# Performance work log

Measured on AMD Instinct MI355X. Metric: run time of the kernel, lower is better.

Reference implementation:

```python
import jax, jax.numpy as jnp
import numpy as np

B_NW, N, DIM, NH, DH, HID, NW, WH = 2048, 64, 512, 16, 32, 384, 64, 8
EPS = 1e-12  # F.normalize eps

def _rel_coords_log(wh, ww):
    # torch.cartesian_prod order: i (rows) outer, j (cols) inner
    ii, jj = np.meshgrid(np.arange(wh), np.arange(ww), indexing='ij')
    coords = np.stack([ii.ravel(), jj.ravel()], axis=-1).astype(np.float32)  # [N,2]
    rel = coords[:, None, :] - coords[None, :, :]                            # [N,N,2]
    return (np.sign(rel) * np.log1p(np.abs(rel))).astype(np.float32)

def setup_inputs() -> dict:
    key = jax.random.key(0)
    ks = jax.random.split(key, 9)
    s = 0.02
    inner = NH * DH
    return {
        'x': jax.random.normal(ks[0], (B_NW, N, DIM), jnp.float32),
        'mask': jax.random.normal(ks[1], (NW, N, N), jnp.float32),
        'w_qkv': jax.random.normal(ks[2], (DIM, 3 * inner), jnp.float32) * s,
        'tau': jnp.ones((1, NH, 1, 1), jnp.float32),
        'mlp_w1': jax.random.normal(ks[3], (2, HID), jnp.float32) * s,
        'mlp_b1': jnp.zeros((HID,), jnp.float32),
        'mlp_w2': jax.random.normal(ks[4], (HID, NH), jnp.float32) * s,
        'mlp_b2': jnp.zeros((NH,), jnp.float32),
        'w_out': jax.random.normal(ks[5], (inner, DIM), jnp.float32) * s,
        'b_out': jnp.zeros((DIM,), jnp.float32),
        'rel_log': jnp.asarray(_rel_coords_log(WH, WH)),
    }

def reference(x, mask, w_qkv, tau, mlp_w1, mlp_b1, mlp_w2, mlp_b2, w_out, b_out, rel_log):
    b, n, _ = x.shape
    qkv = x @ w_qkv                                   # [b, n, 3*nh*dh]
    qkv = qkv.reshape(b, n, 3, NH, DH)
    q, k, v = (jnp.transpose(qkv[:, :, i], (0, 2, 1, 3)) for i in range(3))  # [b, nh, n, dh]
    # cosine attention: L2-normalize q and k along head dim
    q = q / jnp.maximum(jnp.linalg.norm(q, axis=-1, keepdims=True), EPS)
    k = k / jnp.maximum(jnp.linalg.norm(k, axis=-1, keepdims=True), EPS)
    sim = jnp.einsum('bhid,bhjd->bhij', q, k) * tau   # learned temperature
    # relative position bias via meta MLP: [N,N,2] -> [N,N,nh]
    bias = jax.nn.relu(rel_log @ mlp_w1 + mlp_b1) @ mlp_w2 + mlp_b2
    sim = sim + jnp.transpose(bias, (2, 0, 1))[None]  # [1, nh, N, N]
    nw = mask.shape[0]
    sim = sim.reshape(b // nw, nw, NH, n, n) + mask[None, :, None]
    sim = sim.reshape(b, NH, n, n)
    attn = jax.nn.softmax(sim, axis=-1)
    out = jnp.einsum('bhij,bhjd->bhid', attn, v)
    out = jnp.transpose(out, (0, 2, 1, 3)).reshape(b, n, NH * DH)
    return out @ w_out + b_out
```

## Files before the change

### kernel.cpp

```cpp
#include <hip/hip_runtime.h>
#include <hip/hip_bf16.h>


typedef __bf16 bf16;
typedef __bf16 v4bf __attribute__((ext_vector_type(4)));
typedef __bf16 v8bf __attribute__((ext_vector_type(8)));
typedef float  v4f  __attribute__((ext_vector_type(4)));

__global__ void convert_x_kernel(const float* __restrict__ x, bf16* __restrict__ xbf) {
    const int stride = gridDim.x * 256;
    for (size_t idx = blockIdx.x * 256 + threadIdx.x; idx < 8388608; idx += stride) {
        const float4* xv = (const float4*)x;
        float4 v0 = xv[idx * 2];
        float4 v1 = xv[idx * 2 + 1];
        v8bf o = { (bf16)v0.x, (bf16)v0.y, (bf16)v0.z, (bf16)v0.w,
                   (bf16)v1.x, (bf16)v1.y, (bf16)v1.z, (bf16)v1.w };
        *(v8bf*)(xbf + idx * 8) = o;
    }
}

__global__ void convert_w_kernel(const float* __restrict__ wqkv, const float* __restrict__ wout,
                                 bf16* __restrict__ Wt, bf16* __restrict__ WoT) {
    int idx = blockIdx.x * 256 + threadIdx.x;
    Wt[idx] = (bf16)wqkv[(idx & 511) * 1536 + (idx >> 9)];
    if (idx < 262144) WoT[idx] = (bf16)wout[(idx & 511) * 512 + (idx >> 9)];
}

__global__ void bias_kernel(const float* __restrict__ rel_log, const float* __restrict__ w1,
                            const float* __restrict__ b1, const float* __restrict__ w2,
                            const float* __restrict__ b2, float* __restrict__ bias) {
    int p = blockIdx.x * 256 + threadIdx.x;
    float ra = rel_log[p * 2 + 0];
    float rb = rel_log[p * 2 + 1];
    float acc[16];
    #pragma unroll
    for (int t = 0; t < 16; ++t) acc[t] = 0.f;
    for (int kk = 0; kk < 384; ++kk) {
        float hv = fmaxf(ra * w1[kk] + rb * w1[384 + kk] + b1[kk], 0.f);
        #pragma unroll
        for (int t = 0; t < 16; ++t) acc[t] += hv * w2[kk * 16 + t];
    }
    #pragma unroll
    for (int t = 0; t < 16; ++t) bias[t * 4096 + p] = acc[t] + b2[t];
}

__global__ void comb_kernel(const float* __restrict__ bias, const float* __restrict__ mask,
                            float* __restrict__ comb) {
    int idx = blockIdx.x * 256 + threadIdx.x;
    int t = idx & 4095, wh = idx >> 12;
    int w = wh >> 4, h = wh & 15;
    int ji = t >> 8, rem = t & 255;
    int j = ji >> 2, i = ji & 3;
    int q16 = rem >> 2, r = t & 3;
    int lq = q16 >> 4, lm = q16 & 15;
    int p = (i * 16 + lm) * 64 + j * 16 + lq * 4 + r;
    comb[idx] = bias[h * 4096 + p] + mask[w * 4096 + p];
}

__global__ __launch_bounds__(256) void qkv_gemm_kernel(
    const bf16* __restrict__ xbf,
    const bf16* __restrict__ Wt,
    bf16* __restrict__ q_ws, bf16* __restrict__ k_ws, bf16* __restrict__ v_ws)
{
    __shared__ alignas(16) bf16 Alds[2][128 * 32];
    __shared__ alignas(16) bf16 Blds[2][128 * 32];
    const int bid = blockIdx.x, nwg = gridDim.x;
    const int wid = (bid & 7) * (nwg >> 3) + (bid >> 3);
    const int nb = wid % 12, mb = wid / 12;

    const int t = threadIdx.x;
    const int wv = t >> 6, lane = t & 63, lq = lane >> 4, lm = lane & 15;
    const int wr = wv >> 1, wc = wv & 1;

    const char* aBase = (const char*)xbf + (size_t)mb * 128 * 1024;
    const char* bBase = (const char*)Wt + (size_t)nb * 128 * 1024;

    auto stage = [&](int buf, int kt) {
        #pragma unroll
        for (int p = 0; p < 2; ++p) {
            int idx = (p * 4 + wv) * 1024 + lane * 16;
            int row = idx >> 6, kb = idx & 63;
            __builtin_amdgcn_global_load_lds(
                (const __attribute__((address_space(1))) void*)(aBase + (size_t)row * 1024 + kt * 64 + kb),
                (__attribute__((address_space(3))) void*)((char*)Alds + buf * 8192 + (p * 4 + wv) * 1024),
                16, 0, 0);
            __builtin_amdgcn_global_load_lds(
                (const __attribute__((address_space(1))) void*)(bBase + (size_t)row * 1024 + kt * 64 + kb),
                (__attribute__((address_space(3))) void*)((char*)Blds + buf * 8192 + (p * 4 + wv) * 1024),
                16, 0, 0);
        }
    };

    v4f acc[4][4];
    #pragma unroll
    for (int i = 0; i < 4; ++i)
        #pragma unroll
        for (int j = 0; j < 4; ++j) acc[i][j] = v4f{0.f, 0.f, 0.f, 0.f};

    stage(0, 0);
    #pragma unroll 1
    for (int kt = 0; kt < 16; ++kt) {
        if (kt < 15) {
            stage((kt + 1) & 1, kt + 1);
            asm volatile("s_waitcnt vmcnt(4)" ::: "memory");
        } else {
            asm volatile("s_waitcnt vmcnt(0)" ::: "memory");
        }
        __builtin_amdgcn_s_barrier();
        __builtin_amdgcn_sched_barrier(0);
        const bf16* Ab = &Alds[kt & 1][0];
        const bf16* Bb = &Blds[kt & 1][0];
        v8bf af[4], bfj[4];
        #pragma unroll
        for (int i = 0; i < 4; ++i)
            af[i] = *(const v8bf*)(Ab + (wr * 64 + i * 16 + lm) * 32 + lq * 8);
        #pragma unroll
        for (int j = 0; j < 4; ++j)
            bfj[j] = *(const v8bf*)(Bb + (wc * 64 + j * 16 + lm) * 32 + lq * 8);
        #pragma unroll
        for (int i = 0; i < 4; ++i)
            #pragma unroll
            for (int j = 0; j < 4; ++j)
                acc[i][j] = __builtin_amdgcn_mfma_f32_16x16x32_bf16(af[i], bfj[j], acc[i][j], 0, 0, 0);
        __builtin_amdgcn_s_barrier();
    }

    const int bw = mb * 2 + wr;
    if (nb < 8) {
        bf16* dst = (nb < 4) ? q_ws : k_ws;
        const int hbase = (nb & 3) * 4 + wc * 2;
        #pragma unroll
        for (int tpair = 0; tpair < 2; ++tpair) {
            const int h = hbase + tpair;
            #pragma unroll
            for (int i = 0; i < 4; ++i)
                #pragma unroll
                for (int r = 0; r < 4; ++r) {
                    int n = i * 16 + lq * 4 + r;
                    size_t base = ((size_t)(bw * 16 + h) * 64 + n) * 32;
                    dst[base + lm]      = (bf16)acc[i][2 * tpair][r];
                    dst[base + 16 + lm] = (bf16)acc[i][2 * tpair + 1][r];
                }
        }
    } else {
        #pragma unroll
        for (int j = 0; j < 4; ++j) {
            const int h = (nb - 8) * 4 + wc * 2 + (j >> 1);
            const int dh = (j & 1) * 16 + lm;
            #pragma unroll
            for (int i = 0; i < 4; ++i) {
                v4bf pv = { (bf16)acc[i][j][0], (bf16)acc[i][j][1],
                            (bf16)acc[i][j][2], (bf16)acc[i][j][3] };
                *(v4bf*)(v_ws + ((size_t)(bw * 16 + h) * 32 + dh) * 64 + i * 16 + lq * 4) = pv;
            }
        }
    }
}

__global__ __launch_bounds__(256) void attn_kernel(
    const bf16* __restrict__ q_ws,
    const bf16* __restrict__ k_ws,
    const bf16* __restrict__ v_ws,
    const float* __restrict__ comb,
    const float* __restrict__ tau,
    int wofs,
    bf16* __restrict__ attn_out)
{
    __shared__ alignas(16) bf16 P_all[4][64 * 72];
    const int blk = blockIdx.x;
    const int b = blk >> 2, g = blk & 3;
    const int tid = threadIdx.x;
    const int wv = tid >> 6, lane = tid & 63, lq = lane >> 4, lm = lane & 15;
    const int h = g * 4 + wv;
    const v4f z4 = {0.f, 0.f, 0.f, 0.f};

    bf16* P = P_all[wv];
    const size_t qk_base = (size_t)(b * 16 + h) * 64 * 32;
    const float* comb_hw = comb + ((size_t)(((wofs + b) & 63) * 16 + h)) * 4096
                                + (lq * 16 + lm) * 4;
    const float tau_h = tau[h];

    v8bf qf[4], kf[4];
    #pragma unroll
    for (int i = 0; i < 4; ++i)
        qf[i] = *(const v8bf*)(q_ws + qk_base + (i * 16 + lm) * 32 + lq * 8);
    #pragma unroll
    for (int j = 0; j < 4; ++j)
        kf[j] = *(const v8bf*)(k_ws + qk_base + (j * 16 + lm) * 32 + lq * 8);

    #pragma unroll
    for (int i = 0; i < 4; ++i) {
        float a = 0.f;
        #pragma unroll
        for (int e = 0; e < 8; ++e) { float f = (float)qf[i][e]; a = fmaf(f, f, a); }
        a += __shfl_xor(a, 16); a += __shfl_xor(a, 32);
        float sc = tau_h / fmaxf(sqrtf(a), 1e-12f);
        #pragma unroll
        for (int e = 0; e < 8; ++e) qf[i][e] = (bf16)((float)qf[i][e] * sc);
    }
    #pragma unroll
    for (int j = 0; j < 4; ++j) {
        float a = 0.f;
        #pragma unroll
        for (int e = 0; e < 8; ++e) { float f = (float)kf[j][e]; a = fmaf(f, f, a); }
        a += __shfl_xor(a, 16); a += __shfl_xor(a, 32);
        float sc = 1.0f / fmaxf(sqrtf(a), 1e-12f);
        #pragma unroll
        for (int e = 0; e < 8; ++e) kf[j][e] = (bf16)((float)kf[j][e] * sc);
    }

    v4f st[4][4];
    #pragma unroll
    for (int j = 0; j < 4; ++j)
        #pragma unroll
        for (int i = 0; i < 4; ++i)
            st[j][i] = __builtin_amdgcn_mfma_f32_16x16x32_bf16(kf[j], qf[i], z4, 0, 0, 0);

    #pragma unroll
    for (int j = 0; j < 4; ++j)
        #pragma unroll
        for (int i = 0; i < 4; ++i) {
            float4 cv = *(const float4*)(comb_hw + (j * 4 + i) * 256);
            st[j][i][0] += cv.x; st[j][i][1] += cv.y;
            st[j][i][2] += cv.z; st[j][i][3] += cv.w;
        }

    #pragma unroll
    for (int i = 0; i < 4; ++i) {
        float mx = st[0][i][0];
        #pragma unroll
        for (int j = 0; j < 4; ++j)
            #pragma unroll
            for (int r = 0; r < 4; ++r) mx = fmaxf(mx, st[j][i][r]);
        mx = fmaxf(mx, __shfl_xor(mx, 16));
        mx = fmaxf(mx, __shfl_xor(mx, 32));
        float sm = 0.f;
        #pragma unroll
        for (int j = 0; j < 4; ++j)
            #pragma unroll
            for (int r = 0; r < 4; ++r) {
                float e = __expf(st[j][i][r] - mx);
                st[j][i][r] = e; sm += e;
            }
        sm += __shfl_xor(sm, 16); sm += __shfl_xor(sm, 32);
        float rcp = 1.0f / sm;
        #pragma unroll
        for (int j = 0; j < 4; ++j) {
            v4bf pv = { (bf16)(st[j][i][0] * rcp), (bf16)(st[j][i][1] * rcp),
                        (bf16)(st[j][i][2] * rcp), (bf16)(st[j][i][3] * rcp) };
            *(v4bf*)(P + (i * 16 + lm) * 72 + j * 16 + lq * 4) = pv;
        }
    }

    const size_t v_base = (size_t)(b * 16 + h) * 32 * 64;
    v4f o[4][2];
    #pragma unroll
    for (int i = 0; i < 4; ++i)
        #pragma unroll
        for (int nt = 0; nt < 2; ++nt) o[i][nt] = z4;
    #pragma unroll
    for (int kk = 0; kk < 2; ++kk) {
        v8bf vf[2], pf[4];
        #pragma unroll
        for (int nt = 0; nt < 2; ++nt)
            vf[nt] = *(const v8bf*)(v_ws + v_base + (nt * 16 + lm) * 64 + kk * 32 + lq * 8);
        #pragma unroll
        for (int i = 0; i < 4; ++i)
            pf[i] = *(const v8bf*)(P + (i * 16 + lm) * 72 + kk * 32 + lq * 8);
        #pragma unroll
        for (int i = 0; i < 4; ++i)
            #pragma unroll
            for (int nt = 0; nt < 2; ++nt)
                o[i][nt] = __builtin_amdgcn_mfma_f32_16x16x32_bf16(pf[i], vf[nt], o[i][nt], 0, 0, 0);
    }
    #pragma unroll
    for (int i = 0; i < 4; ++i)
        #pragma unroll
        for (int nt = 0; nt < 2; ++nt)
            #pragma unroll
            for (int r = 0; r < 4; ++r)
                attn_out[(size_t)(b * 64 + i * 16 + lq * 4 + r) * 512 + h * 32 + nt * 16 + lm] =
                    (bf16)o[i][nt][r];
}

__global__ __launch_bounds__(256) void proj_gemm_kernel(
    const bf16* __restrict__ A,
    const bf16* __restrict__ Bt,
    const float* __restrict__ b_out,
    float* __restrict__ out)
{
    __shared__ alignas(16) bf16 Alds[2][128 * 32];
    __shared__ alignas(16) bf16 Blds[2][128 * 32];
    const int bid = blockIdx.x;
    const int wid = (bid & 7) * 512 + (bid >> 3);
    const int mb = wid >> 2, nb = wid & 3;
    const int tid = threadIdx.x;
    const int wv = tid >> 6, lane = tid & 63, lq = lane >> 4, lm = lane & 15;
    const int wr = wv >> 1, wc = wv & 1;

    const char* aBase = (const char*)A + (size_t)mb * 128 * 1024;
    const char* bBase = (const char*)Bt + (size_t)nb * 128 * 1024;

    auto stage = [&](int buf, int kt) {
        #pragma unroll
        for (int p = 0; p < 2; ++p) {
            int idx = (p * 4 + wv) * 1024 + lane * 16;
            int row = idx >> 6, kb = idx & 63;
            __builtin_amdgcn_global_load_lds(
                (const __attribute__((address_space(1))) void*)(aBase + (size_t)row * 1024 + kt * 64 + kb),
                (__attribute__((address_space(3))) void*)((char*)Alds + buf * 8192 + (p * 4 + wv) * 1024),
                16, 0, 0);
            __builtin_amdgcn_global_load_lds(
                (const __attribute__((address_space(1))) void*)(bBase + (size_t)row * 1024 + kt * 64 + kb),
                (__attribute__((address_space(3))) void*)((char*)Blds + buf * 8192 + (p * 4 + wv) * 1024),
                16, 0, 0);
        }
    };

    v4f acc[4][4];
    #pragma unroll
    for (int i = 0; i < 4; ++i)
        #pragma unroll
        for (int j = 0; j < 4; ++j) acc[i][j] = v4f{0.f, 0.f, 0.f, 0.f};

    stage(0, 0);
    #pragma unroll 1
    for (int kt = 0; kt < 16; ++kt) {
        if (kt < 15) {
            stage((kt + 1) & 1, kt + 1);
            asm volatile("s_waitcnt vmcnt(4)" ::: "memory");
        } else {
            asm volatile("s_waitcnt vmcnt(0)" ::: "memory");
        }
        __builtin_amdgcn_s_barrier();
        __builtin_amdgcn_sched_barrier(0);
        const bf16* Ab = &Alds[kt & 1][0];
        const bf16* Bb = &Blds[kt & 1][0];
        v8bf af[4], bfj[4];
        #pragma unroll
        for (int i = 0; i < 4; ++i)
            af[i] = *(const v8bf*)(Ab + (wr * 64 + i * 16 + lm) * 32 + lq * 8);
        #pragma unroll
        for (int j = 0; j < 4; ++j)
            bfj[j] = *(const v8bf*)(Bb + (wc * 64 + j * 16 + lm) * 32 + lq * 8);
        #pragma unroll
        for (int i = 0; i < 4; ++i)
            #pragma unroll
            for (int j = 0; j < 4; ++j)
                acc[i][j] = __builtin_amdgcn_mfma_f32_16x16x32_bf16(af[i], bfj[j], acc[i][j], 0, 0, 0);
        __builtin_amdgcn_s_barrier();
    }

    #pragma unroll
    for (int j = 0; j < 4; ++j) {
        int col = nb * 128 + wc * 64 + j * 16 + lm;
        float bo = b_out[col];
        #pragma unroll
        for (int i = 0; i < 4; ++i)
            #pragma unroll
            for (int r = 0; r < 4; ++r)
                out[(size_t)(mb * 128 + wr * 64 + i * 16 + lq * 4 + r) * 512 + col] = acc[i][j][r] + bo;
    }
}

extern "C" void kernel_launch(void* const* d_in, const int* in_sizes, int n_in,
                              void* d_out, int out_size, void* d_ws, size_t ws_size,
                              hipStream_t stream) {
    (void)in_sizes; (void)n_in; (void)out_size;
    const float* x       = (const float*)d_in[0];
    const float* mask    = (const float*)d_in[1];
    const float* w_qkv   = (const float*)d_in[2];
    const float* tau     = (const float*)d_in[3];
    const float* mlp_w1  = (const float*)d_in[4];
    const float* mlp_b1  = (const float*)d_in[5];
    const float* mlp_w2  = (const float*)d_in[6];
    const float* mlp_b2  = (const float*)d_in[7];
    const float* w_out   = (const float*)d_in[8];
    const float* b_out   = (const float*)d_in[9];
    const float* rel_log = (const float*)d_in[10];
    float* out = (float*)d_out;

    char* ws = (char*)d_ws;
    bf16*  Wt     = (bf16*)(ws);
    bf16*  WoT    = (bf16*)(ws + 1572864);
    float* bias   = (float*)(ws + 2097152);
    float* comb   = (float*)(ws + 2359296);
    bf16*  shared = (bf16*)(ws + 19136512);
    char*  qkv_base = ws + 153354240;

    size_t avail = (ws_size > 153354240ULL) ? ws_size - 153354240ULL : 0;
    int W = 2048;
    while (W > 128 && (size_t)W * 196608ULL > avail) W >>= 1;
    const size_t qkbuf = (size_t)W * 65536;
    bf16* qb = (bf16*)qkv_base;
    bf16* kb = (bf16*)(qkv_base + qkbuf);
    bf16* vb = (bf16*)(qkv_base + 2 * qkbuf);

    convert_w_kernel<<<3072, 256, 0, stream>>>(w_qkv, w_out, Wt, WoT);
    bias_kernel<<<16, 256, 0, stream>>>(rel_log, mlp_w1, mlp_b1, mlp_w2, mlp_b2, bias);
    comb_kernel<<<16384, 256, 0, stream>>>(bias, mask, comb);
    convert_x_kernel<<<2048, 256, 0, stream>>>(x, shared);

    const int nchunk = 2048 / W;
    for (int c = 0; c < nchunk; ++c) {
        bf16* slice = shared + (size_t)c * W * 64 * 512;
        qkv_gemm_kernel<<<6 * W, 256, 0, stream>>>(slice, Wt, qb, kb, vb);
        attn_kernel<<<4 * W, 256, 0, stream>>>(qb, kb, vb, comb, tau, c * W, slice);
    }
    proj_gemm_kernel<<<4096, 256, 0, stream>>>(shared, WoT, b_out, out);
}
```

Measured before the change: 751.5 us.

## Enlarge GEMM tiles to 256x256 with 8 waves and swizzled LDS layout

Both the QKV and output-projection GEMMs move from 128x128 tiles with 4 waves to 256x256 tiles with 8 waves, each wave computing a 128x64 sub-tile. The LDS staging adds an XOR swizzle so the fragment reads avoid bank conflicts. Larger tiles raise arithmetic intensity and cut redundant global loads of A and B. In exchange the kernels use more registers and LDS, allow only one workgroup per CU, and launch fewer workgroups, which may hurt latency hiding.

```diff
diff --git a/kernel.cpp b/kernel.cpp
--- a/kernel.cpp
+++ b/kernel.cpp
@@ -57,45 +57,65 @@
     comb[idx] = bias[h * 4096 + p] + mask[w * 4096 + p];
 }
 
-__global__ __launch_bounds__(256) void qkv_gemm_kernel(
+__device__ __forceinline__ int swz(int o) { return o ^ (((o >> 7) & 7) << 4); }
+
+__global__ __launch_bounds__(512, 1) void qkv_gemm_kernel(
     const bf16* __restrict__ xbf,
     const bf16* __restrict__ Wt,
     bf16* __restrict__ q_ws, bf16* __restrict__ k_ws, bf16* __restrict__ v_ws)
 {
-    __shared__ alignas(16) bf16 Alds[2][128 * 32];
-    __shared__ alignas(16) bf16 Blds[2][128 * 32];
+    __shared__ alignas(16) char Alds[2][16384];
+    __shared__ alignas(16) char Blds[2][16384];
     const int bid = blockIdx.x, nwg = gridDim.x;
     const int wid = (bid & 7) * (nwg >> 3) + (bid >> 3);
-    const int nb = wid % 12, mb = wid / 12;
+    const int nb = wid % 6, mb = wid / 6;
 
     const int t = threadIdx.x;
     const int wv = t >> 6, lane = t & 63, lq = lane >> 4, lm = lane & 15;
-    const int wr = wv >> 1, wc = wv & 1;
-
-    const char* aBase = (const char*)xbf + (size_t)mb * 128 * 1024;
-    const char* bBase = (const char*)Wt + (size_t)nb * 128 * 1024;
+    const int wr = wv >> 2, wc = wv & 3;
+
+    const char* aBase = (const char*)xbf + (size_t)mb * 256 * 1024;
+    const char* bBase = (const char*)Wt + (size_t)nb * 256 * 1024;
+
+    int so[2], srow[2], scol[2];
+    #pragma unroll
+    for (int p = 0; p < 2; ++p) {
+        so[p] = p * 8192 + t * 16;
+        int s = swz(so[p]);
+        srow[p] = s >> 6; scol[p] = s & 63;
+    }
 
     auto stage = [&](int buf, int kt) {
         #pragma unroll
         for (int p = 0; p < 2; ++p) {
-            int idx = (p * 4 + wv) * 1024 + lane * 16;
-            int row = idx >> 6, kb = idx & 63;
             __builtin_amdgcn_global_load_lds(
-                (const __attribute__((address_space(1))) void*)(aBase + (size_t)row * 1024 + kt * 64 + kb),
-                (__attribute__((address_space(3))) void*)((char*)Alds + buf * 8192 + (p * 4 + wv) * 1024),
+                (const __attribute__((address_space(1))) void*)(aBase + (size_t)srow[p] * 1024 + kt * 64 + scol[p]),
+                (__attribute__((address_space(3))) void*)(&Alds[buf][0] + (wv * 1024 + (t & 63) * 16) + (so[p] & 8192)),
                 16, 0, 0);
             __builtin_amdgcn_global_load_lds(
-                (const __attribute__((address_space(1))) void*)(bBase + (size_t)row * 1024 + kt * 64 + kb),
-                (__attribute__((address_space(3))) void*)((char*)Blds + buf * 8192 + (p * 4 + wv) * 1024),
+                (const __attribute__((address_space(1))) void*)(bBase + (size_t)srow[p] * 1024 + kt * 64 + scol[p]),
+                (__attribute__((address_space(3))) void*)(&Blds[buf][0] + (wv * 1024 + (t & 63) * 16) + (so[p] & 8192)),
                 16, 0, 0);
         }
     };
 
-    v4f acc[4][4];
-    #pragma unroll
-    for (int i = 0; i < 4; ++i)
+    v4f acc[8][4];
+    #pragma unroll
+    for (int i = 0; i < 8; ++i)
         #pragma unroll
         for (int j = 0; j < 4; ++j) acc[i][j] = v4f{0.f, 0.f, 0.f, 0.f};
+
+    int aoff[8], boff[4];
+    #pragma unroll
+    for (int i = 0; i < 8; ++i) {
+        int row = wr * 128 + i * 16 + lm;
+        aoff[i] = (row * 64 + lq * 16) ^ (((row >> 1) & 7) << 4);
+    }
+    #pragma unroll
+    for (int j = 0; j < 4; ++j) {
+        int row = wc * 64 + j * 16 + lm;
+        boff[j] = (row * 64 + lq * 16) ^ (((row >> 1) & 7) << 4);
+    }
 
     stage(0, 0);
     #pragma unroll 1
@@ -108,50 +128,51 @@
         }
         __builtin_amdgcn_s_barrier();
         __builtin_amdgcn_sched_barrier(0);
-        const bf16* Ab = &Alds[kt & 1][0];
-        const bf16* Bb = &Blds[kt & 1][0];
-        v8bf af[4], bfj[4];
-        #pragma unroll
-        for (int i = 0; i < 4; ++i)
-            af[i] = *(const v8bf*)(Ab + (wr * 64 + i * 16 + lm) * 32 + lq * 8);
-        #pragma unroll
-        for (int j = 0; j < 4; ++j)
-            bfj[j] = *(const v8bf*)(Bb + (wc * 64 + j * 16 + lm) * 32 + lq * 8);
-        #pragma unroll
-        for (int i = 0; i < 4; ++i)
+        const char* Ab = &Alds[kt & 1][0];
+        const char* Bb = &Blds[kt & 1][0];
+        v8bf af[8], bfj[4];
+        #pragma unroll
+        for (int i = 0; i < 8; ++i) af[i] = *(const v8bf*)(Ab + aoff[i]);
+        #pragma unroll
+        for (int j = 0; j < 4; ++j) bfj[j] = *(const v8bf*)(Bb + boff[j]);
+        #pragma unroll
+        for (int i = 0; i < 8; ++i)
             #pragma unroll
             for (int j = 0; j < 4; ++j)
                 acc[i][j] = __builtin_amdgcn_mfma_f32_16x16x32_bf16(af[i], bfj[j], acc[i][j], 0, 0, 0);
         __builtin_amdgcn_s_barrier();
     }
 
-    const int bw = mb * 2 + wr;
-    if (nb < 8) {
-        bf16* dst = (nb < 4) ? q_ws : k_ws;
-        const int hbase = (nb & 3) * 4 + wc * 2;
+    if (nb < 4) {
+        bf16* dst = (nb < 2) ? q_ws : k_ws;
         #pragma unroll
         for (int tpair = 0; tpair < 2; ++tpair) {
-            const int h = hbase + tpair;
-            #pragma unroll
-            for (int i = 0; i < 4; ++i)
+            const int h = (nb & 1) * 8 + wc * 2 + tpair;
+            #pragma unroll
+            for (int i = 0; i < 8; ++i) {
+                const int bw = mb * 4 + wr * 2 + (i >> 2);
                 #pragma unroll
                 for (int r = 0; r < 4; ++r) {
-                    int n = i * 16 + lq * 4 + r;
+                    int n = (i & 3) * 16 + lq * 4 + r;
                     size_t base = ((size_t)(bw * 16 + h) * 64 + n) * 32;
                     dst[base + lm]      = (bf16)acc[i][2 * tpair][r];
                     dst[base + 16 + lm] = (bf16)acc[i][2 * tpair + 1][r];
                 }
+            }
         }
     } else {
         #pragma unroll
         for (int j = 0; j < 4; ++j) {
-            const int h = (nb - 8) * 4 + wc * 2 + (j >> 1);
+            const int h = 8 + wc * 2 + (j >> 1);
+            const int h2 = ((nb - 4) & 1) * 8 + wc * 2 + (j >> 1);
             const int dh = (j & 1) * 16 + lm;
-            #pragma unroll
-            for (int i = 0; i < 4; ++i) {
+            (void)h;
+            #pragma unroll
+            for (int i = 0; i < 8; ++i) {
+                const int bw = mb * 4 + wr * 2 + (i >> 2);
                 v4bf pv = { (bf16)acc[i][j][0], (bf16)acc[i][j][1],
                             (bf16)acc[i][j][2], (bf16)acc[i][j][3] };
-                *(v4bf*)(v_ws + ((size_t)(bw * 16 + h) * 32 + dh) * 64 + i * 16 + lq * 4) = pv;
+                *(v4bf*)(v_ws + ((size_t)(bw * 16 + h2) * 32 + dh) * 64 + (i & 3) * 16 + lq * 4) = pv;
             }
         }
     }
@@ -283,45 +304,63 @@
                     (bf16)o[i][nt][r];
 }
 
-__global__ __launch_bounds__(256) void proj_gemm_kernel(
+__global__ __launch_bounds__(512, 1) void proj_gemm_kernel(
     const bf16* __restrict__ A,
     const bf16* __restrict__ Bt,
     const float* __restrict__ b_out,
     float* __restrict__ out)
 {
-    __shared__ alignas(16) bf16 Alds[2][128 * 32];
-    __shared__ alignas(16) bf16 Blds[2][128 * 32];
+    __shared__ alignas(16) char Alds[2][16384];
+    __shared__ alignas(16) char Blds[2][16384];
     const int bid = blockIdx.x;
-    const int wid = (bid & 7) * 512 + (bid >> 3);
-    const int mb = wid >> 2, nb = wid & 3;
-    const int tid = threadIdx.x;
-    const int wv = tid >> 6, lane = tid & 63, lq = lane >> 4, lm = lane & 15;
-    const int wr = wv >> 1, wc = wv & 1;
-
-    const char* aBase = (const char*)A + (size_t)mb * 128 * 1024;
-    const char* bBase = (const char*)Bt + (size_t)nb * 128 * 1024;
+    const int wid = (bid & 7) * 128 + (bid >> 3);
+    const int nb = wid & 1, mb = wid >> 1;
+    const int t = threadIdx.x;
+    const int wv = t >> 6, lane = t & 63, lq = lane >> 4, lm = lane & 15;
+    const int wr = wv >> 2, wc = wv & 3;
+
+    const char* aBase = (const char*)A + (size_t)mb * 256 * 1024;
+    const char* bBase = (const char*)Bt + (size_t)nb * 256 * 1024;
+
+    int so[2], srow[2], scol[2];
+    #pragma unroll
+    for (int p = 0; p < 2; ++p) {
+        so[p] = p * 8192 + t * 16;
+        int s = swz(so[p]);
+        srow[p] = s >> 6; scol[p] = s & 63;
+    }
 
     auto stage = [&](int buf, int kt) {
         #pragma unroll
         for (int p = 0; p < 2; ++p) {
-            int idx = (p * 4 + wv) * 1024 + lane * 16;
-            int row = idx >> 6, kb = idx & 63;
             __builtin_amdgcn_global_load_lds(
-                (const __attribute__((address_space(1))) void*)(aBase + (size_t)row * 1024 + kt * 64 + kb),
-                (__attribute__((address_space(3))) void*)((char*)Alds + buf * 8192 + (p * 4 + wv) * 1024),
+                (const __attribute__((address_space(1))) void*)(aBase + (size_t)srow[p] * 1024 + kt * 64 + scol[p]),
+                (__attribute__((address_space(3))) void*)(&Alds[buf][0] + (wv * 1024 + (t & 63) * 16) + (so[p] & 8192)),
                 16, 0, 0);
             __builtin_amdgcn_global_load_lds(
-                (const __attribute__((address_space(1))) void*)(bBase + (size_t)row * 1024 + kt * 64 + kb),
-                (__attribute__((address_space(3))) void*)((char*)Blds + buf * 8192 + (p * 4 + wv) * 1024),
+                (const __attribute__((address_space(1))) void*)(bBase + (size_t)srow[p] * 1024 + kt * 64 + scol[p]),
+                (__attribute__((address_space(3))) void*)(&Blds[buf][0] + (wv * 1024 + (t & 63) * 16) + (so[p] & 8192)),
                 16, 0, 0);
         }
     };
 
-    v4f acc[4][4];
-    #pragma unroll
-    for (int i = 0; i < 4; ++i)
+    v4f acc[8][4];
+    #pragma unroll
+    for (int i = 0; i < 8; ++i)
         #pragma unroll
         for (int j = 0; j < 4; ++j) acc[i][j] = v4f{0.f, 0.f, 0.f, 0.f};
+
+    int aoff[8], boff[4];
+    #pragma unroll
+    for (int i = 0; i < 8; ++i) {
+        int row = wr * 128 + i * 16 + lm;
+        aoff[i] = (row * 64 + lq * 16) ^ (((row >> 1) & 7) << 4);
+    }
+    #pragma unroll
+    for (int j = 0; j < 4; ++j) {
+        int row = wc * 64 + j * 16 + lm;
+        boff[j] = (row * 64 + lq * 16) ^ (((row >> 1) & 7) << 4);
+    }
 
     stage(0, 0);
     #pragma unroll 1
@@ -334,17 +373,15 @@
         }
         __builtin_amdgcn_s_barrier();
         __builtin_amdgcn_sched_barrier(0);
-        const bf16* Ab = &Alds[kt & 1][0];
-        const bf16* Bb = &Blds[kt & 1][0];
-        v8bf af[4], bfj[4];
-        #pragma unroll
-        for (int i = 0; i < 4; ++i)
-            af[i] = *(const v8bf*)(Ab + (wr * 64 + i * 16 + lm) * 32 + lq * 8);
-        #pragma unroll
-        for (int j = 0; j < 4; ++j)
-            bfj[j] = *(const v8bf*)(Bb + (wc * 64 + j * 16 + lm) * 32 + lq * 8);
-        #pragma unroll
-        for (int i = 0; i < 4; ++i)
+        const char* Ab = &Alds[kt & 1][0];
+        const char* Bb = &Blds[kt & 1][0];
+        v8bf af[8], bfj[4];
+        #pragma unroll
+        for (int i = 0; i < 8; ++i) af[i] = *(const v8bf*)(Ab + aoff[i]);
+        #pragma unroll
+        for (int j = 0; j < 4; ++j) bfj[j] = *(const v8bf*)(Bb + boff[j]);
+        #pragma unroll
+        for (int i = 0; i < 8; ++i)
             #pragma unroll
             for (int j = 0; j < 4; ++j)
                 acc[i][j] = __builtin_amdgcn_mfma_f32_16x16x32_bf16(af[i], bfj[j], acc[i][j], 0, 0, 0);
@@ -353,13 +390,13 @@
 
     #pragma unroll
     for (int j = 0; j < 4; ++j) {
-        int col = nb * 128 + wc * 64 + j * 16 + lm;
+        int col = nb * 256 + wc * 64 + j * 16 + lm;
         float bo = b_out[col];
         #pragma unroll
-        for (int i = 0; i < 4; ++i)
+        for (int i = 0; i < 8; ++i)
             #pragma unroll
             for (int r = 0; r < 4; ++r)
-                out[(size_t)(mb * 128 + wr * 64 + i * 16 + lq * 4 + r) * 512 + col] = acc[i][j][r] + bo;
+                out[(size_t)(mb * 256 + wr * 128 + i * 16 + lq * 4 + r) * 512 + col] = acc[i][j][r] + bo;
     }
 }
 
@@ -404,8 +441,8 @@
     const int nchunk = 2048 / W;
     for (int c = 0; c < nchunk; ++c) {
         bf16* slice = shared + (size_t)c * W * 64 * 512;
-        qkv_gemm_kernel<<<6 * W, 256, 0, stream>>>(slice, Wt, qb, kb, vb);
+        qkv_gemm_kernel<<<(6 * W) / 4, 512, 0, stream>>>(slice, Wt, qb, kb, vb);
         attn_kernel<<<4 * W, 256, 0, stream>>>(qb, kb, vb, comb, tau, c * W, slice);
     }
-    proj_gemm_kernel<<<4096, 256, 0, stream>>>(shared, WoT, b_out, out);
-}
+    proj_gemm_kernel<<<1024, 512, 0, stream>>>(shared, WoT, b_out, out);
+}
```

Measured after the change: 772.8 us. 2.8% more time.

## Fuse fp32-to-bf16 conversion of x into QKV GEMM A-tile staging with swizzled LDS

Applied to the files above, without the earlier changes.

Drops the separate convert_x kernel. The QKV GEMM now reads fp32 x directly into registers, converts it to bf16, and writes it into XOR-swizzled LDS. B tiles keep using global_load_lds, but with a matching swizzle to reduce bank conflicts. This removes a full bf16 write and re-read of x. In exchange, x is read as fp32 once per N-block, which is 12 times, roughly doubling A-side traffic. The software pipelining of A also now uses register prefetch with __syncthreads instead of explicit vmcnt waits.

```diff
diff --git a/kernel.cpp b/kernel.cpp
--- a/kernel.cpp
+++ b/kernel.cpp
@@ -7,17 +7,7 @@
 typedef __bf16 v8bf __attribute__((ext_vector_type(8)));
 typedef float  v4f  __attribute__((ext_vector_type(4)));
 
-__global__ void convert_x_kernel(const float* __restrict__ x, bf16* __restrict__ xbf) {
-    const int stride = gridDim.x * 256;
-    for (size_t idx = blockIdx.x * 256 + threadIdx.x; idx < 8388608; idx += stride) {
-        const float4* xv = (const float4*)x;
-        float4 v0 = xv[idx * 2];
-        float4 v1 = xv[idx * 2 + 1];
-        v8bf o = { (bf16)v0.x, (bf16)v0.y, (bf16)v0.z, (bf16)v0.w,
-                   (bf16)v1.x, (bf16)v1.y, (bf16)v1.z, (bf16)v1.w };
-        *(v8bf*)(xbf + idx * 8) = o;
-    }
-}
+__device__ __forceinline__ int swz(int o) { return o ^ (((o >> 7) & 7) << 4); }
 
 __global__ void convert_w_kernel(const float* __restrict__ wqkv, const float* __restrict__ wout,
                                  bf16* __restrict__ Wt, bf16* __restrict__ WoT) {
@@ -58,12 +48,12 @@
 }
 
 __global__ __launch_bounds__(256) void qkv_gemm_kernel(
-    const bf16* __restrict__ xbf,
+    const float* __restrict__ x,
     const bf16* __restrict__ Wt,
     bf16* __restrict__ q_ws, bf16* __restrict__ k_ws, bf16* __restrict__ v_ws)
 {
-    __shared__ alignas(16) bf16 Alds[2][128 * 32];
-    __shared__ alignas(16) bf16 Blds[2][128 * 32];
+    __shared__ alignas(16) char Alds[2][8192];
+    __shared__ alignas(16) char Blds[2][8192];
     const int bid = blockIdx.x, nwg = gridDim.x;
     const int wid = (bid & 7) * (nwg >> 3) + (bid >> 3);
     const int nb = wid % 12, mb = wid / 12;
@@ -72,24 +62,42 @@
     const int wv = t >> 6, lane = t & 63, lq = lane >> 4, lm = lane & 15;
     const int wr = wv >> 1, wc = wv & 1;
 
-    const char* aBase = (const char*)xbf + (size_t)mb * 128 * 1024;
-    const char* bBase = (const char*)Wt + (size_t)nb * 128 * 1024;
-
-    auto stage = [&](int buf, int kt) {
-        #pragma unroll
-        for (int p = 0; p < 2; ++p) {
-            int idx = (p * 4 + wv) * 1024 + lane * 16;
-            int row = idx >> 6, kb = idx & 63;
+    const int srow = t >> 1, scol = (t & 1) * 16;
+    const float* aptr = x + (size_t)(mb * 128 + srow) * 512 + scol;
+    const int wbyte = srow * 64 + scol * 2;
+    const int wo0 = swz(wbyte), wo1 = swz(wbyte + 16);
+
+    const char* bBase = (const char*)Wt + (size_t)(nb * 128) * 1024;
+    int so[2], brow[2], bcol[2];
+    #pragma unroll
+    for (int p = 0; p < 2; ++p) {
+        so[p] = p * 4096 + t * 16;
+        int s = swz(so[p]);
+        brow[p] = s >> 6; bcol[p] = s & 63;
+    }
+    auto stageB = [&](int buf, int kt) {
+        #pragma unroll
+        for (int p = 0; p < 2; ++p)
             __builtin_amdgcn_global_load_lds(
-                (const __attribute__((address_space(1))) void*)(aBase + (size_t)row * 1024 + kt * 64 + kb),
-                (__attribute__((address_space(3))) void*)((char*)Alds + buf * 8192 + (p * 4 + wv) * 1024),
+                (const __attribute__((address_space(1))) void*)(bBase + (size_t)brow[p] * 1024 + kt * 64 + bcol[p]),
+                (__attribute__((address_space(3))) void*)(&Blds[buf][0] + so[p]),
                 16, 0, 0);
-            __builtin_amdgcn_global_load_lds(
-                (const __attribute__((address_space(1))) void*)(bBase + (size_t)row * 1024 + kt * 64 + kb),
-                (__attribute__((address_space(3))) void*)((char*)Blds + buf * 8192 + (p * 4 + wv) * 1024),
-                16, 0, 0);
-        }
     };
+    auto writeA = [&](int buf, float4 f0, float4 f1, float4 f2, float4 f3) {
+        v8bf a0 = { (bf16)f0.x, (bf16)f0.y, (bf16)f0.z, (bf16)f0.w,
+                    (bf16)f1.x, (bf16)f1.y, (bf16)f1.z, (bf16)f1.w };
+        v8bf a1 = { (bf16)f2.x, (bf16)f2.y, (bf16)f2.z, (bf16)f2.w,
+                    (bf16)f3.x, (bf16)f3.y, (bf16)f3.z, (bf16)f3.w };
+        *(v8bf*)(&Alds[buf][0] + wo0) = a0;
+        *(v8bf*)(&Alds[buf][0] + wo1) = a1;
+    };
+
+    int aoff[4], boff[4];
+    #pragma unroll
+    for (int i = 0; i < 4; ++i) {
+        aoff[i] = swz((wr * 64 + i * 16 + lm) * 64 + lq * 16);
+        boff[i] = swz((wc * 64 + i * 16 + lm) * 64 + lq * 16);
+    }
 
     v4f acc[4][4];
     #pragma unroll
@@ -97,32 +105,35 @@
         #pragma unroll
         for (int j = 0; j < 4; ++j) acc[i][j] = v4f{0.f, 0.f, 0.f, 0.f};
 
-    stage(0, 0);
+    {
+        const float4* ap = (const float4*)aptr;
+        float4 f0 = ap[0], f1 = ap[1], f2 = ap[2], f3 = ap[3];
+        stageB(0, 0);
+        writeA(0, f0, f1, f2, f3);
+        __syncthreads();
+    }
+
     #pragma unroll 1
     for (int kt = 0; kt < 16; ++kt) {
+        const int cur = kt & 1;
+        float4 f0, f1, f2, f3;
         if (kt < 15) {
-            stage((kt + 1) & 1, kt + 1);
-            asm volatile("s_waitcnt vmcnt(4)" ::: "memory");
-        } else {
-            asm volatile("s_waitcnt vmcnt(0)" ::: "memory");
-        }
-        __builtin_amdgcn_s_barrier();
-        __builtin_amdgcn_sched_barrier(0);
-        const bf16* Ab = &Alds[kt & 1][0];
-        const bf16* Bb = &Blds[kt & 1][0];
+            const float4* ap = (const float4*)(aptr + (kt + 1) * 32);
+            f0 = ap[0]; f1 = ap[1]; f2 = ap[2]; f3 = ap[3];
+            stageB(cur ^ 1, kt + 1);
+        }
         v8bf af[4], bfj[4];
         #pragma unroll
-        for (int i = 0; i < 4; ++i)
-            af[i] = *(const v8bf*)(Ab + (wr * 64 + i * 16 + lm) * 32 + lq * 8);
-        #pragma unroll
-        for (int j = 0; j < 4; ++j)
-            bfj[j] = *(const v8bf*)(Bb + (wc * 64 + j * 16 + lm) * 32 + lq * 8);
+        for (int i = 0; i < 4; ++i) af[i] = *(const v8bf*)(&Alds[cur][0] + aoff[i]);
+        #pragma unroll
+        for (int j = 0; j < 4; ++j) bfj[j] = *(const v8bf*)(&Blds[cur][0] + boff[j]);
         #pragma unroll
         for (int i = 0; i < 4; ++i)
             #pragma unroll
             for (int j = 0; j < 4; ++j)
                 acc[i][j] = __builtin_amdgcn_mfma_f32_16x16x32_bf16(af[i], bfj[j], acc[i][j], 0, 0, 0);
-        __builtin_amdgcn_s_barrier();
+        if (kt < 15) writeA(cur ^ 1, f0, f1, f2, f3);
+        __syncthreads();
     }
 
     const int bw = mb * 2 + wr;
@@ -381,11 +392,11 @@
     float* out = (float*)d_out;
 
     char* ws = (char*)d_ws;
-    bf16*  Wt     = (bf16*)(ws);
-    bf16*  WoT    = (bf16*)(ws + 1572864);
-    float* bias   = (float*)(ws + 2097152);
-    float* comb   = (float*)(ws + 2359296);
-    bf16*  shared = (bf16*)(ws + 19136512);
+    bf16*  Wt       = (bf16*)(ws);
+    bf16*  WoT      = (bf16*)(ws + 1572864);
+    float* bias     = (float*)(ws + 2097152);
+    float* comb     = (float*)(ws + 2359296);
+    bf16*  attn_out = (bf16*)(ws + 19136512);
     char*  qkv_base = ws + 153354240;
 
     size_t avail = (ws_size > 153354240ULL) ? ws_size - 153354240ULL : 0;
@@ -399,13 +410,13 @@
     convert_w_kernel<<<3072, 256, 0, stream>>>(w_qkv, w_out, Wt, WoT);
     bias_kernel<<<16, 256, 0, stream>>>(rel_log, mlp_w1, mlp_b1, mlp_w2, mlp_b2, bias);
     comb_kernel<<<16384, 256, 0, stream>>>(bias, mask, comb);
-    convert_x_kernel<<<2048, 256, 0, stream>>>(x, shared);
 
     const int nchunk = 2048 / W;
     for (int c = 0; c < nchunk; ++c) {
-        bf16* slice = shared + (size_t)c * W * 64 * 512;
-        qkv_gemm_kernel<<<6 * W, 256, 0, stream>>>(slice, Wt, qb, kb, vb);
-        attn_kernel<<<4 * W, 256, 0, stream>>>(qb, kb, vb, comb, tau, c * W, slice);
-    }
-    proj_gemm_kernel<<<4096, 256, 0, stream>>>(shared, WoT, b_out, out);
-}
+        const float* xc = x + (size_t)c * W * 64 * 512;
+        bf16* aoc = attn_out + (size_t)c * W * 64 * 512;
+        qkv_gemm_kernel<<<6 * W, 256, 0, stream>>>(xc, Wt, qb, kb, vb);
+        attn_kernel<<<4 * W, 256, 0, stream>>>(qb, kb, vb, comb, tau, c * W, aoc);
+    }
+    proj_gemm_kernel<<<4096, 256, 0, stream>>>(attn_out, WoT, b_out, out);
+}
```

Measured after the change: 845.9 us. 12.6% more time.

## Fuse attention with output projection, keeping per-window attention output in LDS

Applied to the files above, without the earlier changes.

The attention kernel now handles all 16 heads of a window in one 512-thread block, with each wave doing two heads. It writes the attention output to a shared-memory tile instead of global memory, then runs the output projection GEMM from that tile against WoT, which is read directly from global/L2. This removes the separate projection kernel and the bf16 attention-output round trip through HBM. In exchange, WoT is re-read by every block without LDS staging, LDS use is large (about 140KB), and occupancy is low.

```diff
diff --git a/kernel.cpp b/kernel.cpp
--- a/kernel.cpp
+++ b/kernel.cpp
@@ -157,209 +157,168 @@
     }
 }
 
-__global__ __launch_bounds__(256) void attn_kernel(
+__global__ __launch_bounds__(512) void attn_proj_kernel(
     const bf16* __restrict__ q_ws,
     const bf16* __restrict__ k_ws,
     const bf16* __restrict__ v_ws,
     const float* __restrict__ comb,
     const float* __restrict__ tau,
+    const bf16* __restrict__ WoT,
+    const float* __restrict__ b_out,
     int wofs,
-    bf16* __restrict__ attn_out)
+    float* __restrict__ out)
 {
-    __shared__ alignas(16) bf16 P_all[4][64 * 72];
-    const int blk = blockIdx.x;
-    const int b = blk >> 2, g = blk & 3;
+    __shared__ alignas(16) bf16 AO[64 * 520];
+    __shared__ alignas(16) bf16 P_all[8][64 * 72];
+    const int b = blockIdx.x;
     const int tid = threadIdx.x;
     const int wv = tid >> 6, lane = tid & 63, lq = lane >> 4, lm = lane & 15;
-    const int h = g * 4 + wv;
     const v4f z4 = {0.f, 0.f, 0.f, 0.f};
-
     bf16* P = P_all[wv];
-    const size_t qk_base = (size_t)(b * 16 + h) * 64 * 32;
-    const float* comb_hw = comb + ((size_t)(((wofs + b) & 63) * 16 + h)) * 4096
-                                + (lq * 16 + lm) * 4;
-    const float tau_h = tau[h];
-
-    v8bf qf[4], kf[4];
+
+    #pragma unroll 1
+    for (int hh = 0; hh < 2; ++hh) {
+        const int h = wv * 2 + hh;
+        const size_t qk_base = (size_t)(b * 16 + h) * 64 * 32;
+        const float* comb_hw = comb + ((size_t)(((wofs + b) & 63) * 16 + h)) * 4096
+                                    + (lq * 16 + lm) * 4;
+        const float tau_h = tau[h];
+
+        v8bf qf[4], kf[4];
+        #pragma unroll
+        for (int i = 0; i < 4; ++i)
+            qf[i] = *(const v8bf*)(q_ws + qk_base + (i * 16 + lm) * 32 + lq * 8);
+        #pragma unroll
+        for (int j = 0; j < 4; ++j)
+            kf[j] = *(const v8bf*)(k_ws + qk_base + (j * 16 + lm) * 32 + lq * 8);
+
+        #pragma unroll
+        for (int i = 0; i < 4; ++i) {
+            float a = 0.f;
+            #pragma unroll
+            for (int e = 0; e < 8; ++e) { float f = (float)qf[i][e]; a = fmaf(f, f, a); }
+            a += __shfl_xor(a, 16); a += __shfl_xor(a, 32);
+            float sc = tau_h / fmaxf(sqrtf(a), 1e-12f);
+            #pragma unroll
+            for (int e = 0; e < 8; ++e) qf[i][e] = (bf16)((float)qf[i][e] * sc);
+        }
+        #pragma unroll
+        for (int j = 0; j < 4; ++j) {
+            float a = 0.f;
+            #pragma unroll
+            for (int e = 0; e < 8; ++e) { float f = (float)kf[j][e]; a = fmaf(f, f, a); }
+            a += __shfl_xor(a, 16); a += __shfl_xor(a, 32);
+            float sc = 1.0f / fmaxf(sqrtf(a), 1e-12f);
+            #pragma unroll
+            for (int e = 0; e < 8; ++e) kf[j][e] = (bf16)((float)kf[j][e] * sc);
+        }
+
+        v4f st[4][4];
+        #pragma unroll
+        for (int j = 0; j < 4; ++j)
+            #pragma unroll
+            for (int i = 0; i < 4; ++i)
+                st[j][i] = __builtin_amdgcn_mfma_f32_16x16x32_bf16(kf[j], qf[i], z4, 0, 0, 0);
+
+        #pragma unroll
+        for (int j = 0; j < 4; ++j)
+            #pragma unroll
+            for (int i = 0; i < 4; ++i) {
+                float4 cv = *(const float4*)(comb_hw + (j * 4 + i) * 256);
+                st[j][i][0] += cv.x; st[j][i][1] += cv.y;
+                st[j][i][2] += cv.z; st[j][i][3] += cv.w;
+            }
+
+        #pragma unroll
+        for (int i = 0; i < 4; ++i) {
+            float mx = st[0][i][0];
+            #pragma unroll
+            for (int j = 0; j < 4; ++j)
+                #pragma unroll
+                for (int r = 0; r < 4; ++r) mx = fmaxf(mx, st[j][i][r]);
+            mx = fmaxf(mx, __shfl_xor(mx, 16));
+            mx = fmaxf(mx, __shfl_xor(mx, 32));
+            float sm = 0.f;
+            #pragma unroll
+            for (int j = 0; j < 4; ++j)
+                #pragma unroll
+                for (int r = 0; r < 4; ++r) {
+                    float e = __expf(st[j][i][r] - mx);
+                    st[j][i][r] = e; sm += e;
+                }
+            sm += __shfl_xor(sm, 16); sm += __shfl_xor(sm, 32);
+            float rcp = 1.0f / sm;
+            #pragma unroll
+            for (int j = 0; j < 4; ++j) {
+                v4bf pv = { (bf16)(st[j][i][0] * rcp), (bf16)(st[j][i][1] * rcp),
+                            (bf16)(st[j][i][2] * rcp), (bf16)(st[j][i][3] * rcp) };
+                *(v4bf*)(P + (i * 16 + lm) * 72 + j * 16 + lq * 4) = pv;
+            }
+        }
+
+        const size_t v_base = (size_t)(b * 16 + h) * 32 * 64;
+        v4f o[4][2];
+        #pragma unroll
+        for (int i = 0; i < 4; ++i)
+            #pragma unroll
+            for (int nt = 0; nt < 2; ++nt) o[i][nt] = z4;
+        #pragma unroll
+        for (int kk = 0; kk < 2; ++kk) {
+            v8bf vf[2], pf[4];
+            #pragma unroll
+            for (int nt = 0; nt < 2; ++nt)
+                vf[nt] = *(const v8bf*)(v_ws + v_base + (nt * 16 + lm) * 64 + kk * 32 + lq * 8);
+            #pragma unroll
+            for (int i = 0; i < 4; ++i)
+                pf[i] = *(const v8bf*)(P + (i * 16 + lm) * 72 + kk * 32 + lq * 8);
+            #pragma unroll
+            for (int i = 0; i < 4; ++i)
+                #pragma unroll
+                for (int nt = 0; nt < 2; ++nt)
+                    o[i][nt] = __builtin_amdgcn_mfma_f32_16x16x32_bf16(pf[i], vf[nt], o[i][nt], 0, 0, 0);
+        }
+        #pragma unroll
+        for (int i = 0; i < 4; ++i)
+            #pragma unroll
+            for (int nt = 0; nt < 2; ++nt)
+                #pragma unroll
+                for (int r = 0; r < 4; ++r)
+                    AO[(i * 16 + lq * 4 + r) * 520 + h * 32 + nt * 16 + lm] = (bf16)o[i][nt][r];
+    }
+
+    __syncthreads();
+
+    v4f acc[4][4];
     #pragma unroll
     for (int i = 0; i < 4; ++i)
-        qf[i] = *(const v8bf*)(q_ws + qk_base + (i * 16 + lm) * 32 + lq * 8);
-    #pragma unroll
-    for (int j = 0; j < 4; ++j)
-        kf[j] = *(const v8bf*)(k_ws + qk_base + (j * 16 + lm) * 32 + lq * 8);
-
-    #pragma unroll
-    for (int i = 0; i < 4; ++i) {
-        float a = 0.f;
-        #pragma unroll
-        for (int e = 0; e < 8; ++e) { float f = (float)qf[i][e]; a = fmaf(f, f, a); }
-        a += __shfl_xor(a, 16); a += __shfl_xor(a, 32);
-        float sc = tau_h / fmaxf(sqrtf(a), 1e-12f);
-        #pragma unroll
-        for (int e = 0; e < 8; ++e) qf[i][e] = (bf16)((float)qf[i][e] * sc);
-    }
-    #pragma unroll
-    for (int j = 0; j < 4; ++j) {
-        float a = 0.f;
-        #pragma unroll
-        for (int e = 0; e < 8; ++e) { float f = (float)kf[j][e]; a = fmaf(f, f, a); }
-        a += __shfl_xor(a, 16); a += __shfl_xor(a, 32);
-        float sc = 1.0f / fmaxf(sqrtf(a), 1e-12f);
-        #pragma unroll
-        for (int e = 0; e < 8; ++e) kf[j][e] = (bf16)((float)kf[j][e] * sc);
-    }
-
-    v4f st[4][4];
-    #pragma unroll
-    for (int j = 0; j < 4; ++j)
-        #pragma unroll
-        for (int i = 0; i < 4; ++i)
-            st[j][i] = __builtin_amdgcn_mfma_f32_16x16x32_bf16(kf[j], qf[i], z4, 0, 0, 0);
-
-    #pragma unroll
-    for (int j = 0; j < 4; ++j)
-        #pragma unroll
-        for (int i = 0; i < 4; ++i) {
-            float4 cv = *(const float4*)(comb_hw + (j * 4 + i) * 256);
-            st[j][i][0] += cv.x; st[j][i][1] += cv.y;
-            st[j][i][2] += cv.z; st[j][i][3] += cv.w;
-        }
-
-    #pragma unroll
-    for (int i = 0; i < 4; ++i) {
-        float mx = st[0][i][0];
-        #pragma unroll
-        for (int j = 0; j < 4; ++j)
-            #pragma unroll
-            for (int r = 0; r < 4; ++r) mx = fmaxf(mx, st[j][i][r]);
-        mx = fmaxf(mx, __shfl_xor(mx, 16));
-        mx = fmaxf(mx, __shfl_xor(mx, 32));
-        float sm = 0.f;
-        #pragma unroll
-        for (int j = 0; j < 4; ++j)
-            #pragma unroll
-            for (int r = 0; r < 4; ++r) {
-                float e = __expf(st[j][i][r] - mx);
-                st[j][i][r] = e; sm += e;
-            }
-        sm += __shfl_xor(sm, 16); sm += __shfl_xor(sm, 32);
-        float rcp = 1.0f / sm;
-        #pragma unroll
-        for (int j = 0; j < 4; ++j) {
-            v4bf pv = { (bf16)(st[j][i][0] * rcp), (bf16)(st[j][i][1] * rcp),
-                        (bf16)(st[j][i][2] * rcp), (bf16)(st[j][i][3] * rcp) };
-            *(v4bf*)(P + (i * 16 + lm) * 72 + j * 16 + lq * 4) = pv;
-        }
-    }
-
-    const size_t v_base = (size_t)(b * 16 + h) * 32 * 64;
-    v4f o[4][2];
-    #pragma unroll
-    for (int i = 0; i < 4; ++i)
-        #pragma unroll
-        for (int nt = 0; nt < 2; ++nt) o[i][nt] = z4;
-    #pragma unroll
-    for (int kk = 0; kk < 2; ++kk) {
-        v8bf vf[2], pf[4];
-        #pragma unroll
-        for (int nt = 0; nt < 2; ++nt)
-            vf[nt] = *(const v8bf*)(v_ws + v_base + (nt * 16 + lm) * 64 + kk * 32 + lq * 8);
-        #pragma unroll
-        for (int i = 0; i < 4; ++i)
-            pf[i] = *(const v8bf*)(P + (i * 16 + lm) * 72 + kk * 32 + lq * 8);
-        #pragma unroll
-        for (int i = 0; i < 4; ++i)
-            #pragma unroll
-            for (int nt = 0; nt < 2; ++nt)
-                o[i][nt] = __builtin_amdgcn_mfma_f32_16x16x32_bf16(pf[i], vf[nt], o[i][nt], 0, 0, 0);
-    }
-    #pragma unroll
-    for (int i = 0; i < 4; ++i)
-        #pragma unroll
-        for (int nt = 0; nt < 2; ++nt)
-            #pragma unroll
-            for (int r = 0; r < 4; ++r)
-                attn_out[(size_t)(b * 64 + i * 16 + lq * 4 + r) * 512 + h * 32 + nt * 16 + lm] =
-                    (bf16)o[i][nt][r];
-}
-
-__global__ __launch_bounds__(256) void proj_gemm_kernel(
-    const bf16* __restrict__ A,
-    const bf16* __restrict__ Bt,
-    const float* __restrict__ b_out,
-    float* __restrict__ out)
-{
-    __shared__ alignas(16) bf16 Alds[2][128 * 32];
-    __shared__ alignas(16) bf16 Blds[2][128 * 32];
-    const int bid = blockIdx.x;
-    const int wid = (bid & 7) * 512 + (bid >> 3);
-    const int mb = wid >> 2, nb = wid & 3;
-    const int tid = threadIdx.x;
-    const int wv = tid >> 6, lane = tid & 63, lq = lane >> 4, lm = lane & 15;
-    const int wr = wv >> 1, wc = wv & 1;
-
-    const char* aBase = (const char*)A + (size_t)mb * 128 * 1024;
-    const char* bBase = (const char*)Bt + (size_t)nb * 128 * 1024;
-
-    auto stage = [&](int buf, int kt) {
-        #pragma unroll
-        for (int p = 0; p < 2; ++p) {
-            int idx = (p * 4 + wv) * 1024 + lane * 16;
-            int row = idx >> 6, kb = idx & 63;
-            __builtin_amdgcn_global_load_lds(
-                (const __attribute__((address_space(1))) void*)(aBase + (size_t)row * 1024 + kt * 64 + kb),
-                (__attribute__((address_space(3))) void*)((char*)Alds + buf * 8192 + (p * 4 + wv) * 1024),
-                16, 0, 0);
-            __builtin_amdgcn_global_load_lds(
-                (const __attribute__((address_space(1))) void*)(bBase + (size_t)row * 1024 + kt * 64 + kb),
-                (__attribute__((address_space(3))) void*)((char*)Blds + buf * 8192 + (p * 4 + wv) * 1024),
-                16, 0, 0);
-        }
-    };
-
-    v4f acc[4][4];
-    #pragma unroll
-    for (int i = 0; i < 4; ++i)
         #pragma unroll
         for (int j = 0; j < 4; ++j) acc[i][j] = v4f{0.f, 0.f, 0.f, 0.f};
 
-    stage(0, 0);
-    #pragma unroll 1
-    for (int kt = 0; kt < 16; ++kt) {
-        if (kt < 15) {
-            stage((kt + 1) & 1, kt + 1);
-            asm volatile("s_waitcnt vmcnt(4)" ::: "memory");
-        } else {
-            asm volatile("s_waitcnt vmcnt(0)" ::: "memory");
-        }
-        __builtin_amdgcn_s_barrier();
-        __builtin_amdgcn_sched_barrier(0);
-        const bf16* Ab = &Alds[kt & 1][0];
-        const bf16* Bb = &Blds[kt & 1][0];
+    #pragma unroll 2
+    for (int kc = 0; kc < 16; ++kc) {
         v8bf af[4], bfj[4];
         #pragma unroll
-        for (int i = 0; i < 4; ++i)
-            af[i] = *(const v8bf*)(Ab + (wr * 64 + i * 16 + lm) * 32 + lq * 8);
-        #pragma unroll
-        for (int j = 0; j < 4; ++j)
-            bfj[j] = *(const v8bf*)(Bb + (wc * 64 + j * 16 + lm) * 32 + lq * 8);
+        for (int j = 0; j < 4; ++j)
+            bfj[j] = *(const v8bf*)(WoT + (size_t)(wv * 64 + j * 16 + lm) * 512 + kc * 32 + lq * 8);
+        #pragma unroll
+        for (int i = 0; i < 4; ++i)
+            af[i] = *(const v8bf*)(AO + (i * 16 + lm) * 520 + kc * 32 + lq * 8);
         #pragma unroll
         for (int i = 0; i < 4; ++i)
             #pragma unroll
             for (int j = 0; j < 4; ++j)
                 acc[i][j] = __builtin_amdgcn_mfma_f32_16x16x32_bf16(af[i], bfj[j], acc[i][j], 0, 0, 0);
-        __builtin_amdgcn_s_barrier();
     }
 
     #pragma unroll
     for (int j = 0; j < 4; ++j) {
-        int col = nb * 128 + wc * 64 + j * 16 + lm;
-        float bo = b_out[col];
+        const int col = wv * 64 + j * 16 + lm;
+        const float bo = b_out[col];
         #pragma unroll
         for (int i = 0; i < 4; ++i)
             #pragma unroll
             for (int r = 0; r < 4; ++r)
-                out[(size_t)(mb * 128 + wr * 64 + i * 16 + lq * 4 + r) * 512 + col] = acc[i][j][r] + bo;
+                out[(size_t)(b * 64 + i * 16 + lq * 4 + r) * 512 + col] = acc[i][j][r] + bo;
     }
 }
 
@@ -385,7 +344,7 @@
     bf16*  WoT    = (bf16*)(ws + 1572864);
     float* bias   = (float*)(ws + 2097152);
     float* comb   = (float*)(ws + 2359296);
-    bf16*  shared = (bf16*)(ws + 19136512);
+    bf16*  xbf    = (bf16*)(ws + 19136512);
     char*  qkv_base = ws + 153354240;
 
     size_t avail = (ws_size > 153354240ULL) ? ws_size - 153354240ULL : 0;
@@ -399,13 +358,13 @@
     convert_w_kernel<<<3072, 256, 0, stream>>>(w_qkv, w_out, Wt, WoT);
     bias_kernel<<<16, 256, 0, stream>>>(rel_log, mlp_w1, mlp_b1, mlp_w2, mlp_b2, bias);
     comb_kernel<<<16384, 256, 0, stream>>>(bias, mask, comb);
-    convert_x_kernel<<<2048, 256, 0, stream>>>(x, shared);
+    convert_x_kernel<<<2048, 256, 0, stream>>>(x, xbf);
 
     const int nchunk = 2048 / W;
     for (int c = 0; c < nchunk; ++c) {
-        bf16* slice = shared + (size_t)c * W * 64 * 512;
+        bf16* slice = xbf + (size_t)c * W * 64 * 512;
         qkv_gemm_kernel<<<6 * W, 256, 0, stream>>>(slice, Wt, qb, kb, vb);
-        attn_kernel<<<4 * W, 256, 0, stream>>>(qb, kb, vb, comb, tau, c * W, slice);
-    }
-    proj_gemm_kernel<<<4096, 256, 0, stream>>>(shared, WoT, b_out, out);
-}
+        attn_proj_kernel<<<W, 512, 0, stream>>>(qb, kb, vb, comb, tau, WoT, b_out,
+                                                c * W, out + (size_t)c * W * 64 * 512);
+    }
+}
```

Result: no change. 745.4 us (-0.8%).
